# Optimization experiments

Hardware: AMD Instinct MI355X
Metric: run time of the kernel (lower is better)

The kernel has to match this reference:

```python
import jax, jax.numpy as jnp
import numpy as np

N_NODES = 100000
N_EDGES = 800000
EMB = 256
NUM_LAYER = 5
BN_EPS = 1e-5


def setup_inputs() -> dict:
    key = jax.random.key(0)
    ks = jax.random.split(key, 16)
    s = 0.05
    return {
        "x_atom": jax.random.randint(ks[0], (N_NODES,), 0, 120, dtype=jnp.int32),
        "x_chir": jax.random.randint(ks[1], (N_NODES,), 0, 3, dtype=jnp.int32),
        "edge_src": jax.random.randint(ks[2], (N_EDGES,), 0, N_NODES, dtype=jnp.int32),
        "edge_dst": jax.random.randint(ks[3], (N_EDGES,), 0, N_NODES, dtype=jnp.int32),
        "ea_type": jax.random.randint(ks[4], (N_EDGES,), 0, 6, dtype=jnp.int32),
        "ea_dir": jax.random.randint(ks[5], (N_EDGES,), 0, 3, dtype=jnp.int32),
        "x_emb1": jax.random.normal(ks[6], (120, EMB), jnp.float32) * s,
        "x_emb2": jax.random.normal(ks[7], (3, EMB), jnp.float32) * s,
        "edge_emb1": jax.random.normal(ks[8], (NUM_LAYER, 6, EMB), jnp.float32) * s,
        "edge_emb2": jax.random.normal(ks[9], (NUM_LAYER, 3, EMB), jnp.float32) * s,
        "W1": jax.random.normal(ks[10], (NUM_LAYER, EMB, 2 * EMB), jnp.float32) * s,
        "b1": jnp.zeros((NUM_LAYER, 2 * EMB), jnp.float32),
        "W2": jax.random.normal(ks[11], (NUM_LAYER, 2 * EMB, EMB), jnp.float32) * s,
        "b2": jnp.zeros((NUM_LAYER, EMB), jnp.float32),
        "gamma": jnp.ones((NUM_LAYER, EMB), jnp.float32),
        "beta": jnp.zeros((NUM_LAYER, EMB), jnp.float32),
    }


def _gnn_forward(x_emb1, x_emb2, edge_emb1, edge_emb2, W1, b1, W2, b2, gamma, beta,
                 x_atom, x_chir, edge_src, edge_dst, ea_type, ea_dir):
    N = x_atom.shape[0]
    # node input embedding
    h = x_emb1[x_atom] + x_emb2[x_chir]  # [N, D]
    # add self loops (edge attr [4, 0] per original code)
    loop = jnp.arange(N, dtype=edge_src.dtype)
    src = jnp.concatenate([edge_src, loop])
    dst = jnp.concatenate([edge_dst, loop])
    et = jnp.concatenate([ea_type, jnp.full((N,), 4, dtype=ea_type.dtype)])
    ed = jnp.concatenate([ea_dir, jnp.zeros((N,), dtype=ea_dir.dtype)])
    L = W1.shape[0]
    for l in range(L):
        ee = edge_emb1[l][et] + edge_emb2[l][ed]          # [E+N, D]
        msg = h[src] + ee                                  # gather + edge embed
        agg = jax.ops.segment_sum(msg, dst, num_segments=N)  # scatter-add
        # 2-layer MLP update
        hl = jax.nn.relu(agg @ W1[l] + b1[l]) @ W2[l] + b2[l]
        # BatchNorm1d (training mode: biased batch statistics)
        mean = jnp.mean(hl, axis=0)
        var = jnp.mean(jnp.square(hl - mean), axis=0)
        hl = (hl - mean) * (gamma[l] / jnp.sqrt(var + BN_EPS)) + beta[l]
        # dropout with drop_ratio=0.0 is identity; relu on all but last layer
        if l < L - 1:
            hl = jax.nn.relu(hl)
        h = hl
    return h  # JK='last'


def reference(x_atom, x_chir, edge_src, edge_dst, ea_type, ea_dir,
              x_emb1, x_emb2, edge_emb1, edge_emb2, W1, b1, W2, b2, gamma, beta):
    return _gnn_forward(x_emb1, x_emb2, edge_emb1, edge_emb2, W1, b1, W2, b2,
                        gamma, beta, x_atom, x_chir, edge_src, edge_dst, ea_type, ea_dir)
```

## Files before the change

kernel.cpp:

```cpp
#include <hip/hip_runtime.h>
#include <cstdint>

typedef float f32x4 __attribute__((ext_vector_type(4)));
typedef __bf16 bf16x8 __attribute__((ext_vector_type(8)));
typedef unsigned short ushort4v __attribute__((ext_vector_type(4)));
typedef unsigned short u16;
typedef unsigned int u32;

__device__ __forceinline__ u16 f2bf(float f) {
  u32 u = __builtin_bit_cast(u32, f);
  u32 r = (u + 0x7fffu + ((u >> 16) & 1u)) >> 16;
  return (u16)r;
}

__device__ __forceinline__ float4 b2f4(ushort4v v) {
  float4 o;
  o.x = __builtin_bit_cast(float, (u32)v[0] << 16);
  o.y = __builtin_bit_cast(float, (u32)v[1] << 16);
  o.z = __builtin_bit_cast(float, (u32)v[2] << 16);
  o.w = __builtin_bit_cast(float, (u32)v[3] << 16);
  return o;
}

__device__ __forceinline__ void gload_lds16(const void* g, void* lds) {
  __builtin_amdgcn_global_load_lds(
      (const __attribute__((address_space(1))) u32*)g,
      (__attribute__((address_space(3))) u32*)lds,
      16, 0, 0);
}

__global__ __launch_bounds__(256) void k_cast_weights(
    const float* __restrict__ W1, const float* __restrict__ W2,
    u16* __restrict__ w1t, u16* __restrict__ w2t) {
  const int PER = 5 * 512 * 256;
  int idx = blockIdx.x * 256 + threadIdx.x;
  if (idx < PER) {
    int l = idx / (512 * 256);
    int rem = idx % (512 * 256);
    int n = rem / 256, k = rem % 256;
    w1t[idx] = f2bf(W1[l * 131072 + k * 512 + n]);
  } else if (idx < 2 * PER) {
    int j = idx - PER;
    int l = j / (256 * 512);
    int rem = j % (256 * 512);
    int n = rem / 512, k = rem % 512;
    w2t[j] = f2bf(W2[l * 131072 + k * 256 + n]);
  }
}

__global__ __launch_bounds__(256) void k_node_init(
    const int* __restrict__ xa, const int* __restrict__ xc,
    const float* __restrict__ e1, const float* __restrict__ e2,
    u16* __restrict__ h, int N) {
  int idx = blockIdx.x * 256 + threadIdx.x;
  if (idx >= N * 64) return;
  int node = idx >> 6, c = (idx & 63) * 4;
  int a = xa[node], ch = xc[node];
  float4 v1 = *(const float4*)&e1[a * 256 + c];
  float4 v2 = *(const float4*)&e2[ch * 256 + c];
  ushort4v o;
  o[0] = f2bf(v1.x + v2.x); o[1] = f2bf(v1.y + v2.y);
  o[2] = f2bf(v1.z + v2.z); o[3] = f2bf(v1.w + v2.w);
  *(ushort4v*)&h[(size_t)node * 256 + c] = o;
}

__global__ __launch_bounds__(256) void k_deg_count(
    const int* __restrict__ dst, int* __restrict__ deg, int E) {
  int e = blockIdx.x * 256 + threadIdx.x;
  if (e < E) atomicAdd(&deg[dst[e]], 1);
}

__global__ __launch_bounds__(256) void k_scan1(
    const int* __restrict__ deg, int* __restrict__ rp,
    int* __restrict__ bsum, int N) {
  __shared__ int s[256];
  int i = blockIdx.x * 256 + threadIdx.x;
  int v = (i < N) ? deg[i] : 0;
  s[threadIdx.x] = v;
  __syncthreads();
#pragma unroll
  for (int off = 1; off < 256; off <<= 1) {
    int t = (threadIdx.x >= off) ? s[threadIdx.x - off] : 0;
    __syncthreads();
    s[threadIdx.x] += t;
    __syncthreads();
  }
  if (i < N) rp[i] = s[threadIdx.x] - v;
  if (threadIdx.x == 255) bsum[blockIdx.x] = s[255];
}

__global__ __launch_bounds__(512) void k_scan2(
    const int* __restrict__ bsum, int* __restrict__ bexcl, int B) {
  __shared__ int s[512];
  int v = (threadIdx.x < B) ? bsum[threadIdx.x] : 0;
  s[threadIdx.x] = v;
  __syncthreads();
#pragma unroll
  for (int off = 1; off < 512; off <<= 1) {
    int t = (threadIdx.x >= off) ? s[threadIdx.x - off] : 0;
    __syncthreads();
    s[threadIdx.x] += t;
    __syncthreads();
  }
  if (threadIdx.x < B) bexcl[threadIdx.x] = s[threadIdx.x] - v;
}

__global__ __launch_bounds__(256) void k_scan3(
    int* __restrict__ rp, const int* __restrict__ bexcl,
    int* __restrict__ cur, int N, int E) {
  int i = blockIdx.x * 256 + threadIdx.x;
  if (i < N) {
    int v = rp[i] + bexcl[blockIdx.x];
    rp[i] = v;
    cur[i] = v;
  }
  if (i == 0) rp[N] = E;
}

__global__ __launch_bounds__(256) void k_fill(
    const int* __restrict__ src, const int* __restrict__ dst,
    const int* __restrict__ et, const int* __restrict__ ed,
    int* __restrict__ cur, u32* __restrict__ adj, int E) {
  int e = blockIdx.x * 256 + threadIdx.x;
  if (e >= E) return;
  int pos = atomicAdd(&cur[dst[e]], 1);
  adj[pos] = (u32)src[e] | ((u32)et[e] << 17) | ((u32)ed[e] << 20);
}

__global__ __launch_bounds__(256) void k_gather(
    const u16* __restrict__ h, const int* __restrict__ rp,
    const u32* __restrict__ adj, const float* __restrict__ ee1,
    const float* __restrict__ ee2, u16* __restrict__ aggb, int N) {
  int node = blockIdx.x * 4 + (threadIdx.x >> 6);
  if (node >= N) return;
  int lane = threadIdx.x & 63;
  int c = lane * 4;
  float4 a0 = b2f4(*(const ushort4v*)&h[(size_t)node * 256 + c]);
  float4 a1 = make_float4(0.f, 0.f, 0.f, 0.f);
  float4 a2 = a1, a3 = a1;
  u32 tcA = 0, tcB = 0;
  int beg = rp[node], end = rp[node + 1];
  int i = beg;
  for (; i + 4 <= end; i += 4) {
    u32 p0 = adj[i], p1 = adj[i + 1], p2 = adj[i + 2], p3 = adj[i + 3];
    float4 v0 = b2f4(*(const ushort4v*)&h[(size_t)(p0 & 0x1FFFF) * 256 + c]);
    float4 v1 = b2f4(*(const ushort4v*)&h[(size_t)(p1 & 0x1FFFF) * 256 + c]);
    float4 v2 = b2f4(*(const ushort4v*)&h[(size_t)(p2 & 0x1FFFF) * 256 + c]);
    float4 v3 = b2f4(*(const ushort4v*)&h[(size_t)(p3 & 0x1FFFF) * 256 + c]);
    a0.x += v0.x; a0.y += v0.y; a0.z += v0.z; a0.w += v0.w;
    a1.x += v1.x; a1.y += v1.y; a1.z += v1.z; a1.w += v1.w;
    a2.x += v2.x; a2.y += v2.y; a2.z += v2.z; a2.w += v2.w;
    a3.x += v3.x; a3.y += v3.y; a3.z += v3.z; a3.w += v3.w;
#pragma unroll
    for (int u = 0; u < 4; ++u) {
      u32 p = (u == 0) ? p0 : (u == 1) ? p1 : (u == 2) ? p2 : p3;
      u32 t = (p >> 17) & 7, r = (p >> 20) & 3;
      tcA += (t < 4) ? (1u << (t * 8)) : 0u;
      tcB += ((t == 4) ? 1u : 0u) + ((r == 0) ? 256u : 0u) +
             ((r == 1) ? 65536u : 0u);
    }
  }
  for (; i < end; ++i) {
    u32 p = adj[i];
    float4 v = b2f4(*(const ushort4v*)&h[(size_t)(p & 0x1FFFF) * 256 + c]);
    a0.x += v.x; a0.y += v.y; a0.z += v.z; a0.w += v.w;
    u32 t = (p >> 17) & 7, r = (p >> 20) & 3;
    tcA += (t < 4) ? (1u << (t * 8)) : 0u;
    tcB += ((t == 4) ? 1u : 0u) + ((r == 0) ? 256u : 0u) +
           ((r == 1) ? 65536u : 0u);
  }
  int deg = end - beg;
  int i0 = tcA & 255, i1 = (tcA >> 8) & 255, i2 = (tcA >> 16) & 255,
      i3 = (tcA >> 24) & 255;
  int i4 = (int)(tcB & 255) + 1;
  int r0 = (int)((tcB >> 8) & 255) + 1;
  int r1 = (int)((tcB >> 16) & 255);
  int i5 = deg - i0 - i1 - i2 - i3 - (i4 - 1);
  int r2 = deg - (r0 - 1) - r1;
  float ct[6], cr[3];
  ct[0] = (float)i0; ct[1] = (float)i1; ct[2] = (float)i2;
  ct[3] = (float)i3; ct[4] = (float)i4; ct[5] = (float)i5;
  cr[0] = (float)r0; cr[1] = (float)r1; cr[2] = (float)r2;

  float ax = a0.x + a1.x + a2.x + a3.x;
  float ay = a0.y + a1.y + a2.y + a3.y;
  float az = a0.z + a1.z + a2.z + a3.z;
  float aw = a0.w + a1.w + a2.w + a3.w;
#pragma unroll
  for (int t = 0; t < 6; ++t) {
    float4 e = *(const float4*)&ee1[t * 256 + c];
    ax += ct[t] * e.x; ay += ct[t] * e.y;
    az += ct[t] * e.z; aw += ct[t] * e.w;
  }
#pragma unroll
  for (int r = 0; r < 3; ++r) {
    float4 e = *(const float4*)&ee2[r * 256 + c];
    ax += cr[r] * e.x; ay += cr[r] * e.y;
    az += cr[r] * e.z; aw += cr[r] * e.w;
  }
  ushort4v o;
  o[0] = f2bf(ax); o[1] = f2bf(ay); o[2] = f2bf(az); o[3] = f2bf(aw);
  *(ushort4v*)&aggb[(size_t)node * 256 + c] = o;
}

template <int K, int NC, int OUTMODE, bool STATS>
__global__ __launch_bounds__(512) void k_gemm(
    const u16* __restrict__ A, const u16* __restrict__ Bt,
    const float* __restrict__ bias, void* __restrict__ outp,
    float* __restrict__ st, int M) {
  constexpr int NSTEP = K / 32;
  __shared__ u16 As[2][128 * 32];
  __shared__ u16 Bs[2][256 * 32];
  const int tid = threadIdx.x;
  const int lane = tid & 63;
  const int wv = tid >> 6;
  const int wrow = wv >> 2, wcol = wv & 3;
  const int m0 = blockIdx.x * 128;
  const int n0 = blockIdx.y * 256;
  const int fr = lane & 15;
  const int kg = lane >> 4;

  f32x4 acc[4][4];
#pragma unroll
  for (int m = 0; m < 4; ++m)
#pragma unroll
    for (int n = 0; n < 4; ++n) acc[m][n] = (f32x4){0.f, 0.f, 0.f, 0.f};

  auto stage = [&](int k0, int b) {
    {
      const int cidx = tid;
      const int lidx = cidx ^ ((cidx >> 3) & 7);
      int row = lidx >> 2, kcol = lidx & 3;
      int ar = m0 + row;
      if (ar >= M) ar = M - 1;
      gload_lds16(A + (size_t)ar * K + k0 + kcol * 8,
                  (char*)As[b] + (tid & ~63) * 16);
    }
#pragma unroll
    for (int j = 0; j < 2; ++j) {
      const int cidx = j * 512 + tid;
      const int lidx = cidx ^ ((cidx >> 3) & 7);
      int row = lidx >> 2, kcol = lidx & 3;
      gload_lds16(Bt + (size_t)(n0 + row) * K + k0 + kcol * 8,
                  (char*)Bs[b] + (j * 512 + (tid & ~63)) * 16);
    }
  };

  stage(0, 0);
  for (int ks = 0; ks < NSTEP; ++ks) {
    const int b = ks & 1;
    if (ks + 1 < NSTEP) {
      stage((ks + 1) * 32, b ^ 1);
      asm volatile("s_waitcnt vmcnt(3)" ::: "memory");
    } else {
      asm volatile("s_waitcnt vmcnt(0)" ::: "memory");
    }
    __builtin_amdgcn_sched_barrier(0);
    __builtin_amdgcn_s_barrier();
    __builtin_amdgcn_sched_barrier(0);
    bf16x8 af[4], bf[4];
#pragma unroll
    for (int m = 0; m < 4; ++m) {
      int row = wrow * 64 + m * 16 + fr;
      int off = ((row << 2) + kg) ^ ((row >> 1) & 7);
      af[m] = *(const bf16x8*)((const char*)As[b] + (off << 4));
    }
#pragma unroll
    for (int n = 0; n < 4; ++n) {
      int row = wcol * 64 + n * 16 + fr;
      int off = ((row << 2) + kg) ^ ((row >> 1) & 7);
      bf[n] = *(const bf16x8*)((const char*)Bs[b] + (off << 4));
    }
#pragma unroll
    for (int m = 0; m < 4; ++m)
#pragma unroll
      for (int n = 0; n < 4; ++n)
        acc[m][n] = __builtin_amdgcn_mfma_f32_16x16x32_bf16(af[m], bf[n],
                                                            acc[m][n], 0, 0, 0);
    __builtin_amdgcn_sched_barrier(0);
    __builtin_amdgcn_s_barrier();
  }

  float* sst = (float*)As;
  if (STATS) {
    __syncthreads();
    sst[tid] = 0.f;
    __syncthreads();
  }

  const int rb = kg * 4;
  float s[4], s2[4];
#pragma unroll
  for (int n = 0; n < 4; ++n) { s[n] = 0.f; s2[n] = 0.f; }
#pragma unroll
  for (int m = 0; m < 4; ++m) {
#pragma unroll
    for (int n = 0; n < 4; ++n) {
      const int col = n0 + wcol * 64 + n * 16 + fr;
      const float bv = bias[col];
#pragma unroll
      for (int j = 0; j < 4; ++j) {
        const int row = m0 + wrow * 64 + m * 16 + rb + j;
        if (row < M) {
          float v = acc[m][n][j] + bv;
          if (OUTMODE == 2) {
            v = fmaxf(v, 0.f);
            ((u16*)outp)[(size_t)row * NC + col] = f2bf(v);
          } else {
            ((float*)outp)[(size_t)row * NC + col] = v;
          }
          if (STATS) {
            s[n] += v;
            s2[n] += v * v;
          }
        }
      }
    }
  }
  if (STATS) {
#pragma unroll
    for (int n = 0; n < 4; ++n) {
      s[n] += __shfl_xor(s[n], 16);
      s[n] += __shfl_xor(s[n], 32);
      s2[n] += __shfl_xor(s2[n], 16);
      s2[n] += __shfl_xor(s2[n], 32);
    }
    if (lane < 16) {
#pragma unroll
      for (int n = 0; n < 4; ++n) {
        const int col = wcol * 64 + n * 16 + fr;
        atomicAdd(&sst[col], s[n]);
        atomicAdd(&sst[256 + col], s2[n]);
      }
    }
    __syncthreads();
    unsafeAtomicAdd(&st[tid], sst[tid]);
  }
}

template <bool BF16RELU>
__global__ __launch_bounds__(256) void k_bn_apply(
    const float* __restrict__ hl, const float* __restrict__ stats,
    const float* __restrict__ gamma, const float* __restrict__ beta,
    int l, float invN, void* __restrict__ out, int N) {
  int idx = blockIdx.x * 256 + threadIdx.x;
  if (idx >= N * 64) return;
  int c = (idx & 63) * 4;
  float4 sum = *(const float4*)&stats[c];
  float4 ssq = *(const float4*)&stats[256 + c];
  float4 g = *(const float4*)&gamma[l * 256 + c];
  float4 bt = *(const float4*)&beta[l * 256 + c];
  float4 mean = make_float4(sum.x * invN, sum.y * invN, sum.z * invN,
                            sum.w * invN);
  float4 sc, sh;
  sc.x = g.x * rsqrtf(ssq.x * invN - mean.x * mean.x + 1e-5f);
  sc.y = g.y * rsqrtf(ssq.y * invN - mean.y * mean.y + 1e-5f);
  sc.z = g.z * rsqrtf(ssq.z * invN - mean.z * mean.z + 1e-5f);
  sc.w = g.w * rsqrtf(ssq.w * invN - mean.w * mean.w + 1e-5f);
  sh.x = bt.x - mean.x * sc.x; sh.y = bt.y - mean.y * sc.y;
  sh.z = bt.z - mean.z * sc.z; sh.w = bt.w - mean.w * sc.w;
  float4 v = *(const float4*)&hl[(size_t)idx * 4];
  float4 o = make_float4(v.x * sc.x + sh.x, v.y * sc.y + sh.y,
                         v.z * sc.z + sh.z, v.w * sc.w + sh.w);
  if (BF16RELU) {
    ushort4v ob;
    ob[0] = f2bf(fmaxf(o.x, 0.f)); ob[1] = f2bf(fmaxf(o.y, 0.f));
    ob[2] = f2bf(fmaxf(o.z, 0.f)); ob[3] = f2bf(fmaxf(o.w, 0.f));
    *(ushort4v*)&((u16*)out)[(size_t)idx * 4] = ob;
  } else {
    *(float4*)&((float*)out)[(size_t)idx * 4] = o;
  }
}

extern "C" void kernel_launch(void* const* d_in, const int* in_sizes, int n_in,
                              void* d_out, int out_size, void* d_ws,
                              size_t ws_size, hipStream_t stream) {
  const int* x_atom = (const int*)d_in[0];
  const int* x_chir = (const int*)d_in[1];
  const int* esrc = (const int*)d_in[2];
  const int* edst = (const int*)d_in[3];
  const int* etype = (const int*)d_in[4];
  const int* edir = (const int*)d_in[5];
  const float* x_emb1 = (const float*)d_in[6];
  const float* x_emb2 = (const float*)d_in[7];
  const float* eemb1 = (const float*)d_in[8];
  const float* eemb2 = (const float*)d_in[9];
  const float* W1 = (const float*)d_in[10];
  const float* b1 = (const float*)d_in[11];
  const float* W2 = (const float*)d_in[12];
  const float* b2 = (const float*)d_in[13];
  const float* gamma = (const float*)d_in[14];
  const float* beta = (const float*)d_in[15];

  const int N = in_sizes[0];
  const int E = in_sizes[2];

  char* ws = (char*)d_ws;
  size_t off = 0;
  char* bufA = ws + off; off += (size_t)N * 1024;
  char* bufB = ws + off; off += (size_t)N * 1024;
  u16* aggb = (u16*)(ws + off); off += (size_t)N * 256 * 2;
  u16* w1t = (u16*)(ws + off); off += (size_t)5 * 512 * 256 * 2;
  u16* w2t = (u16*)(ws + off); off += (size_t)5 * 256 * 512 * 2;
  int* rp = (int*)(ws + off); off += (size_t)(N + 1) * 4;
  int* degcur = (int*)(ws + off); off += (size_t)N * 4;
  int* bsum = (int*)(ws + off); off += 512 * 4;
  int* bexcl = (int*)(ws + off); off += 512 * 4;
  u32* adj = (u32*)(ws + off); off += (size_t)E * 4;
  float* statsAll = (float*)(ws + off); off += 5 * 1024 * 4;

  const int gN64 = (N * 64 + 255) / 256;
  const int gE = (E + 255) / 256;
  const int B1 = (N + 255) / 256;
  const int NB128 = (N + 127) / 128;

  u16* hn = (u16*)bufA;
  u16* interb = (u16*)bufA;
  float* hl = (float*)bufB;

  hipMemsetAsync(degcur, 0, (size_t)N * 4, stream);
  hipMemsetAsync(statsAll, 0, 5 * 1024 * 4, stream);
  k_deg_count<<<gE, 256, 0, stream>>>(edst, degcur, E);
  k_scan1<<<B1, 256, 0, stream>>>(degcur, rp, bsum, N);
  k_scan2<<<1, 512, 0, stream>>>(bsum, bexcl, B1);
  k_scan3<<<B1, 256, 0, stream>>>(rp, bexcl, degcur, N, E);
  k_fill<<<gE, 256, 0, stream>>>(esrc, edst, etype, edir, degcur, adj, E);
  k_cast_weights<<<(2 * 5 * 512 * 256 + 255) / 256, 256, 0, stream>>>(W1, W2,
                                                                      w1t, w2t);
  k_node_init<<<gN64, 256, 0, stream>>>(x_atom, x_chir, x_emb1, x_emb2, hn, N);

  for (int l = 0; l < 5; ++l) {
    const float* ee1 = eemb1 + (size_t)l * 6 * 256;
    const float* ee2 = eemb2 + (size_t)l * 3 * 256;
    float* st = statsAll + l * 1024;

    k_gather<<<(N + 3) / 4, 256, 0, stream>>>(hn, rp, adj, ee1, ee2, aggb, N);
    k_gemm<256, 512, 2, false><<<dim3(NB128, 2), 512, 0, stream>>>(
        aggb, w1t + (size_t)l * 512 * 256, b1 + l * 512, interb, nullptr, N);
    k_gemm<512, 256, 0, true><<<dim3(NB128, 1), 512, 0, stream>>>(
        interb, w2t + (size_t)l * 256 * 512, b2 + l * 256, hl, st, N);
    if (l < 4)
      k_bn_apply<true><<<gN64, 256, 0, stream>>>(hl, st, gamma, beta, l,
                                                 1.f / N, hn, N);
    else
      k_bn_apply<false><<<gN64, 256, 0, stream>>>(hl, st, gamma, beta, l,
                                                  1.f / N, d_out, N);
  }
}
```

Before: 1.250 ms.

## Fuse the two MLP GEMMs, keeping the intermediate activation in LDS

Replaces the two separate GEMM launches with one kernel per 128-row tile. It computes relu(agg@W1+b1) into a 128KB LDS buffer, then multiplies by W2 (read directly from global) and accumulates the BatchNorm statistics. This removes the global write and reread of the 512-wide bf16 intermediate and one kernel launch per layer. In exchange the large LDS footprint and 128 accumulator registers limit occupancy to one block per CU, and the second GEMM has no staged prefetch of W2.

After: 1.368 ms. 9.5% more time.

```diff
diff --git a/kernel.cpp b/kernel.cpp
--- a/kernel.cpp
+++ b/kernel.cpp
@@ -203,139 +203,175 @@
   *(ushort4v*)&aggb[(size_t)node * 256 + c] = o;
 }
 
-template <int K, int NC, int OUTMODE, bool STATS>
-__global__ __launch_bounds__(512) void k_gemm(
-    const u16* __restrict__ A, const u16* __restrict__ Bt,
-    const float* __restrict__ bias, void* __restrict__ outp,
+__global__ __launch_bounds__(512, 2) void k_mlp(
+    const u16* __restrict__ aggb, const u16* __restrict__ w1t,
+    const float* __restrict__ b1, const u16* __restrict__ w2t,
+    const float* __restrict__ b2, float* __restrict__ hl,
     float* __restrict__ st, int M) {
-  constexpr int NSTEP = K / 32;
-  __shared__ u16 As[2][128 * 32];
-  __shared__ u16 Bs[2][256 * 32];
+  __shared__ __align__(16) char lds[131072];
+  u16* AsBuf[2] = {(u16*)lds, (u16*)(lds + 8192)};
+  u16* BsBuf[2] = {(u16*)(lds + 16384), (u16*)(lds + 49152)};
+  u16* inter = (u16*)lds;
+
   const int tid = threadIdx.x;
   const int lane = tid & 63;
   const int wv = tid >> 6;
-  const int wrow = wv >> 2, wcol = wv & 3;
+  const int wrow = wv >> 2;
+  const int wcol = wv & 3;
   const int m0 = blockIdx.x * 128;
-  const int n0 = blockIdx.y * 256;
   const int fr = lane & 15;
   const int kg = lane >> 4;
-
-  f32x4 acc[4][4];
-#pragma unroll
-  for (int m = 0; m < 4; ++m)
-#pragma unroll
-    for (int n = 0; n < 4; ++n) acc[m][n] = (f32x4){0.f, 0.f, 0.f, 0.f};
-
-  auto stage = [&](int k0, int b) {
+  const int rb = kg * 4;
+
+  f32x4 acc[4][8];
+#pragma unroll
+  for (int mf = 0; mf < 4; ++mf)
+#pragma unroll
+    for (int nf = 0; nf < 8; ++nf) acc[mf][nf] = (f32x4){0.f, 0.f, 0.f, 0.f};
+
+  auto stageA = [&](int k0, int b) {
     {
       const int cidx = tid;
       const int lidx = cidx ^ ((cidx >> 3) & 7);
       int row = lidx >> 2, kcol = lidx & 3;
       int ar = m0 + row;
       if (ar >= M) ar = M - 1;
-      gload_lds16(A + (size_t)ar * K + k0 + kcol * 8,
-                  (char*)As[b] + (tid & ~63) * 16);
-    }
-#pragma unroll
-    for (int j = 0; j < 2; ++j) {
+      gload_lds16(aggb + (size_t)ar * 256 + k0 + kcol * 8,
+                  (char*)AsBuf[b] + (tid & ~63) * 16);
+    }
+#pragma unroll
+    for (int j = 0; j < 4; ++j) {
       const int cidx = j * 512 + tid;
       const int lidx = cidx ^ ((cidx >> 3) & 7);
       int row = lidx >> 2, kcol = lidx & 3;
-      gload_lds16(Bt + (size_t)(n0 + row) * K + k0 + kcol * 8,
-                  (char*)Bs[b] + (j * 512 + (tid & ~63)) * 16);
+      gload_lds16(w1t + (size_t)row * 256 + k0 + kcol * 8,
+                  (char*)BsBuf[b] + (j * 512 + (tid & ~63)) * 16);
     }
   };
 
-  stage(0, 0);
-  for (int ks = 0; ks < NSTEP; ++ks) {
+  stageA(0, 0);
+  for (int ks = 0; ks < 8; ++ks) {
     const int b = ks & 1;
-    if (ks + 1 < NSTEP) {
-      stage((ks + 1) * 32, b ^ 1);
-      asm volatile("s_waitcnt vmcnt(3)" ::: "memory");
+    if (ks + 1 < 8) {
+      stageA((ks + 1) * 32, b ^ 1);
+      asm volatile("s_waitcnt vmcnt(5)" ::: "memory");
     } else {
       asm volatile("s_waitcnt vmcnt(0)" ::: "memory");
     }
     __builtin_amdgcn_sched_barrier(0);
     __builtin_amdgcn_s_barrier();
     __builtin_amdgcn_sched_barrier(0);
-    bf16x8 af[4], bf[4];
-#pragma unroll
-    for (int m = 0; m < 4; ++m) {
-      int row = wrow * 64 + m * 16 + fr;
+    bf16x8 af[4], bf[8];
+#pragma unroll
+    for (int mf = 0; mf < 4; ++mf) {
+      int row = wrow * 64 + mf * 16 + fr;
       int off = ((row << 2) + kg) ^ ((row >> 1) & 7);
-      af[m] = *(const bf16x8*)((const char*)As[b] + (off << 4));
-    }
-#pragma unroll
-    for (int n = 0; n < 4; ++n) {
-      int row = wcol * 64 + n * 16 + fr;
-      int off = ((row << 2) + kg) ^ ((row >> 1) & 7);
-      bf[n] = *(const bf16x8*)((const char*)Bs[b] + (off << 4));
-    }
-#pragma unroll
-    for (int m = 0; m < 4; ++m)
-#pragma unroll
-      for (int n = 0; n < 4; ++n)
-        acc[m][n] = __builtin_amdgcn_mfma_f32_16x16x32_bf16(af[m], bf[n],
-                                                            acc[m][n], 0, 0, 0);
+      af[mf] = *(const bf16x8*)((const char*)AsBuf[b] + (off << 4));
+    }
+#pragma unroll
+    for (int nf = 0; nf < 8; ++nf) {
+      int brow = wcol * 128 + nf * 16 + fr;
+      int off = ((brow << 2) + kg) ^ ((brow >> 1) & 7);
+      bf[nf] = *(const bf16x8*)((const char*)BsBuf[b] + (off << 4));
+    }
+#pragma unroll
+    for (int mf = 0; mf < 4; ++mf)
+#pragma unroll
+      for (int nf = 0; nf < 8; ++nf)
+        acc[mf][nf] = __builtin_amdgcn_mfma_f32_16x16x32_bf16(af[mf], bf[nf],
+                                                              acc[mf][nf],
+                                                              0, 0, 0);
     __builtin_amdgcn_sched_barrier(0);
     __builtin_amdgcn_s_barrier();
   }
-
-  float* sst = (float*)As;
-  if (STATS) {
-    __syncthreads();
-    sst[tid] = 0.f;
-    __syncthreads();
-  }
-
-  const int rb = kg * 4;
+#pragma unroll
+  for (int mf = 0; mf < 4; ++mf) {
+#pragma unroll
+    for (int nf = 0; nf < 8; ++nf) {
+      const int col = wcol * 128 + nf * 16 + fr;
+      const float bv = b1[col];
+#pragma unroll
+      for (int j = 0; j < 4; ++j) {
+        int row = wrow * 64 + mf * 16 + rb + j;
+        float v = fmaxf(acc[mf][nf][j] + bv, 0.f);
+        int chunk = (row * 64 + (col >> 3)) ^ (row & 7);
+        inter[chunk * 8 + (col & 7)] = f2bf(v);
+      }
+    }
+  }
+  __syncthreads();
+
+  f32x4 acc2[4][4];
+#pragma unroll
+  for (int mf = 0; mf < 4; ++mf)
+#pragma unroll
+    for (int nf = 0; nf < 4; ++nf) acc2[mf][nf] = (f32x4){0.f, 0.f, 0.f, 0.f};
+
+  for (int ks = 0; ks < 16; ++ks) {
+    bf16x8 bf[4], af[4];
+#pragma unroll
+    for (int nf = 0; nf < 4; ++nf) {
+      int brow = wcol * 64 + nf * 16 + fr;
+      bf[nf] = *(const bf16x8*)&w2t[(size_t)brow * 512 + ks * 32 + kg * 8];
+    }
+#pragma unroll
+    for (int mf = 0; mf < 4; ++mf) {
+      int row = wrow * 64 + mf * 16 + fr;
+      int chunk = (row * 64 + ks * 4 + kg) ^ (row & 7);
+      af[mf] = *(const bf16x8*)&inter[chunk * 8];
+    }
+#pragma unroll
+    for (int mf = 0; mf < 4; ++mf)
+#pragma unroll
+      for (int nf = 0; nf < 4; ++nf)
+        acc2[mf][nf] = __builtin_amdgcn_mfma_f32_16x16x32_bf16(af[mf], bf[nf],
+                                                               acc2[mf][nf],
+                                                               0, 0, 0);
+  }
+
+  float* sst = (float*)lds;
+  __syncthreads();
+  sst[tid] = 0.f;
+  __syncthreads();
+
   float s[4], s2[4];
 #pragma unroll
-  for (int n = 0; n < 4; ++n) { s[n] = 0.f; s2[n] = 0.f; }
-#pragma unroll
-  for (int m = 0; m < 4; ++m) {
-#pragma unroll
-    for (int n = 0; n < 4; ++n) {
-      const int col = n0 + wcol * 64 + n * 16 + fr;
-      const float bv = bias[col];
+  for (int nf = 0; nf < 4; ++nf) { s[nf] = 0.f; s2[nf] = 0.f; }
+#pragma unroll
+  for (int mf = 0; mf < 4; ++mf) {
+#pragma unroll
+    for (int nf = 0; nf < 4; ++nf) {
+      const int col = wcol * 64 + nf * 16 + fr;
+      const float bv = b2[col];
 #pragma unroll
       for (int j = 0; j < 4; ++j) {
-        const int row = m0 + wrow * 64 + m * 16 + rb + j;
+        const int row = m0 + wrow * 64 + mf * 16 + rb + j;
         if (row < M) {
-          float v = acc[m][n][j] + bv;
-          if (OUTMODE == 2) {
-            v = fmaxf(v, 0.f);
-            ((u16*)outp)[(size_t)row * NC + col] = f2bf(v);
-          } else {
-            ((float*)outp)[(size_t)row * NC + col] = v;
-          }
-          if (STATS) {
-            s[n] += v;
-            s2[n] += v * v;
-          }
+          float v = acc2[mf][nf][j] + bv;
+          hl[(size_t)row * 256 + col] = v;
+          s[nf] += v;
+          s2[nf] += v * v;
         }
       }
     }
   }
-  if (STATS) {
-#pragma unroll
-    for (int n = 0; n < 4; ++n) {
-      s[n] += __shfl_xor(s[n], 16);
-      s[n] += __shfl_xor(s[n], 32);
-      s2[n] += __shfl_xor(s2[n], 16);
-      s2[n] += __shfl_xor(s2[n], 32);
-    }
-    if (lane < 16) {
-#pragma unroll
-      for (int n = 0; n < 4; ++n) {
-        const int col = wcol * 64 + n * 16 + fr;
-        atomicAdd(&sst[col], s[n]);
-        atomicAdd(&sst[256 + col], s2[n]);
-      }
-    }
-    __syncthreads();
-    unsafeAtomicAdd(&st[tid], sst[tid]);
-  }
+#pragma unroll
+  for (int nf = 0; nf < 4; ++nf) {
+    s[nf] += __shfl_xor(s[nf], 16);
+    s[nf] += __shfl_xor(s[nf], 32);
+    s2[nf] += __shfl_xor(s2[nf], 16);
+    s2[nf] += __shfl_xor(s2[nf], 32);
+  }
+  if (lane < 16) {
+#pragma unroll
+    for (int nf = 0; nf < 4; ++nf) {
+      const int col = wcol * 64 + nf * 16 + fr;
+      atomicAdd(&sst[col], s[nf]);
+      atomicAdd(&sst[256 + col], s2[nf]);
+    }
+  }
+  __syncthreads();
+  unsafeAtomicAdd(&st[tid], sst[tid]);
 }
 
 template <bool BF16RELU>
@@ -415,7 +451,6 @@
   const int NB128 = (N + 127) / 128;
 
   u16* hn = (u16*)bufA;
-  u16* interb = (u16*)bufA;
   float* hl = (float*)bufB;
 
   hipMemsetAsync(degcur, 0, (size_t)N * 4, stream);
@@ -435,10 +470,9 @@
     float* st = statsAll + l * 1024;
 
     k_gather<<<(N + 3) / 4, 256, 0, stream>>>(hn, rp, adj, ee1, ee2, aggb, N);
-    k_gemm<256, 512, 2, false><<<dim3(NB128, 2), 512, 0, stream>>>(
-        aggb, w1t + (size_t)l * 512 * 256, b1 + l * 512, interb, nullptr, N);
-    k_gemm<512, 256, 0, true><<<dim3(NB128, 1), 512, 0, stream>>>(
-        interb, w2t + (size_t)l * 256 * 512, b2 + l * 256, hl, st, N);
+    k_mlp<<<NB128, 512, 0, stream>>>(aggb, w1t + (size_t)l * 131072,
+                                     b1 + l * 512, w2t + (size_t)l * 131072,
+                                     b2 + l * 256, hl, st, N);
     if (l < 4)
       k_bn_apply<true><<<gN64, 256, 0, stream>>>(hl, st, gamma, beta, l,
                                                  1.f / N, hn, N);
```
